# Performance work log

Hardware: AMD Instinct MI355X
Metric: run time of the kernel (lower is better)

## Reference

```python
import jax, jax.numpy as jnp
import numpy as np

BETA = 0.001
VAR_MIN = 1e-7


def setup_inputs() -> dict:
    key = jax.random.key(0)
    ks = jax.random.split(key, 16)
    B, IN, N, Z, S = 2048, 32, 1024, 8, 8
    f32 = jnp.float32
    return {
        "batch": jax.random.normal(ks[0], (B, IN, N, 2), f32),
        "labels": jax.random.randint(ks[1], (B, 1), 0, 2).astype(jnp.int32),
        "eps1": jax.random.normal(ks[2], (B, S, Z), f32),
        "eps2": jax.random.normal(ks[3], (B, S, Z), f32),
        "W1": jax.random.normal(ks[4], (IN, 32), f32) / np.sqrt(IN),
        "b1": jax.random.normal(ks[5], (32,), f32) * 0.01,
        "W2": jax.random.normal(ks[6], (32, 32), f32) / np.sqrt(32),
        "b2": jax.random.normal(ks[7], (32,), f32) * 0.01,
        "Wmu": jax.random.normal(ks[8], (32, Z), f32) / np.sqrt(32),
        "bmu": jax.random.normal(ks[9], (Z,), f32) * 0.01,
        "Wv": jax.random.normal(ks[10], (32, Z), f32) / np.sqrt(32),
        "bv": jax.random.normal(ks[11], (Z,), f32) * 0.01,
        "sw": jax.random.normal(ks[12], (1, 1), f32),
        "sb": jax.random.normal(ks[13], (1,), f32),
    }


def _cal_z(data, W1, b1, W2, b2, Wmu, bmu, Wv, bv):
    # data: [B, IN, N] -> points [B, N, IN]
    x = jnp.transpose(data, (0, 2, 1))
    h = jax.nn.relu(x @ W1 + b1)
    h = jax.nn.relu(h @ W2 + b2)
    mu = h @ Wmu + bmu                    # [B, N, Z]
    var = jax.nn.softplus(h @ Wv + bv)    # [B, N, Z]
    var = jnp.maximum(var, VAR_MIN)
    var_pog = 1.0 / jnp.sum(1.0 / var, axis=1)  # [B, Z]
    # Faithful to torch source: var is reassigned before mu update, so
    # mu = var_pog * sum(mu / var_pog) == sum(mu) over the N axis.
    mu_pog = jnp.sum(mu, axis=1)                # [B, Z]
    return mu_pog, var_pog


def _kl(mu, var):
    # KL(N(mu, sqrt(var)) || N(0, 1)), elementwise, then mean
    return jnp.mean(-0.5 * jnp.log(var) + 0.5 * (var + mu * mu) - 0.5)


def reference(batch, labels, eps1, eps2, W1, b1, W2, b2, Wmu, bmu, Wv, bv, sw, sb):
    mu1, var1 = _cal_z(batch[:, :, :, 0], W1, b1, W2, b2, Wmu, bmu, Wv, bv)
    mu2, var2 = _cal_z(batch[:, :, :, 1], W1, b1, W2, b2, Wmu, bmu, Wv, bv)

    kl = (_kl(mu1, var1) + _kl(mu2, var2)) * BETA

    # rsample: mu + sigma * eps, [B, S, Z]
    z1 = mu1[:, None, :] + jnp.sqrt(var1)[:, None, :] * eps1
    z2 = mu2[:, None, :] + jnp.sqrt(var2)[:, None, :] * eps2

    # pairwise distances over the S x S sample grid: [B, S, S]
    diff = z1[:, :, None, :] - z2[:, None, :, :]
    dist = jnp.sqrt(jnp.sum(diff * diff, axis=-1))

    a = jax.nn.softplus(sw[0, 0])
    p = jax.nn.sigmoid(-a * dist + sb[0])
    loss1 = -jnp.log(p)
    loss_1 = jnp.mean(loss1, axis=(1, 2), keepdims=False)[:, None]  # [B, 1]
    # Faithful bug in torch source: loss0 is never assigned, stays zero,
    # so the (1 - labels) term contributes nothing.
    labels_f = labels.astype(loss_1.dtype)
    soft = jnp.mean(loss_1 * labels_f)

    return kl + soft
```

## Files before the change

### kernel.cpp

```cpp
#include <hip/hip_runtime.h>
#include <hip/hip_bf16.h>

#define B_   2048
#define N_   1024
#define BETA 0.001f
#define VAR_MIN 1e-7f

#define PTS   64
#define NSTG  (N_ / PTS)
#define RF    128
#define NBUF  3

typedef __attribute__((ext_vector_type(8))) short  bf16x8;
typedef __attribute__((ext_vector_type(4))) float  f32x4;

__device__ __forceinline__ unsigned short f2bf_u(float x) {
    __hip_bfloat16 h = __float2bfloat16(x);
    return __builtin_bit_cast(unsigned short, h);
}
__device__ __forceinline__ float softplus_cheap(float x) {
    float sp = __logf(1.f + __expf(x));
    return x > 15.f ? x : sp;
}
__device__ __forceinline__ float rcp_fast(float x) {
    return __builtin_amdgcn_rcpf(x);
}
__device__ __forceinline__ float softplus_ref(float x) {
    return x > 20.f ? x : log1pf(expf(x));
}

__device__ __forceinline__ int kperm(int k) {
    return 4 * (k >> 3) + (k & 3) + 16 * ((k >> 2) & 1);
}

extern "C" __global__ void hib_prep(const float* __restrict__ W1,
                                    const float* __restrict__ W2,
                                    const float* __restrict__ Wmu,
                                    const float* __restrict__ Wv,
                                    unsigned short* __restrict__ wf)
{
    const int l = threadIdx.x;
    const int r = l & 15, kb = l >> 4;
#pragma unroll
    for (int j = 0; j < 8; j++) {
        const int k1 = kb * 8 + j;
        const int kp = kperm(k1);
        wf[(0 * 64 + l) * 8 + j] = f2bf_u(W1[k1 * 32 + r]);
        wf[(1 * 64 + l) * 8 + j] = f2bf_u(W1[k1 * 32 + 16 + r]);
        wf[(2 * 64 + l) * 8 + j] = f2bf_u(W2[kp * 32 + r]);
        wf[(3 * 64 + l) * 8 + j] = f2bf_u(W2[kp * 32 + 16 + r]);
        wf[(4 * 64 + l) * 8 + j] = f2bf_u(r < 8 ? Wmu[kp * 8 + r]
                                                : Wv[kp * 8 + (r - 8)]);
    }
}

__device__ __forceinline__ bf16x8 pack_relu(f32x4 a, f32x4 b) {
    bf16x8 o;
    o[0] = (short)f2bf_u(fmaxf(a[0], 0.f));
    o[1] = (short)f2bf_u(fmaxf(a[1], 0.f));
    o[2] = (short)f2bf_u(fmaxf(a[2], 0.f));
    o[3] = (short)f2bf_u(fmaxf(a[3], 0.f));
    o[4] = (short)f2bf_u(fmaxf(b[0], 0.f));
    o[5] = (short)f2bf_u(fmaxf(b[1], 0.f));
    o[6] = (short)f2bf_u(fmaxf(b[2], 0.f));
    o[7] = (short)f2bf_u(fmaxf(b[3], 0.f));
    return o;
}

__device__ __forceinline__ void red16(f32x4& v) {
#pragma unroll
    for (int off = 8; off; off >>= 1) {
        v[0] += __shfl_down(v[0], off);
        v[1] += __shfl_down(v[1], off);
        v[2] += __shfl_down(v[2], off);
        v[3] += __shfl_down(v[3], off);
    }
}

__device__ __forceinline__ void stage_issue(const float* __restrict__ bbase,
                                            float* __restrict__ ldsbuf,
                                            int st, int wid, int l)
{
    const int sub = l >> 5, lo = l & 31;
#pragma unroll
    for (int q = 0; q < 4; ++q) {
        const int row = wid * 8 + q * 2;
        const float* gs = bbase + (size_t)(row + sub) * (2 * N_) + st * RF + lo * 4;
        __builtin_amdgcn_global_load_lds(
            (const __attribute__((address_space(1))) unsigned int*)gs,
            (__attribute__((address_space(3))) unsigned int*)&ldsbuf[row * RF],
            16, 0, 0);
    }
}

__global__ void __launch_bounds__(256, 3)
hib_mfma(const float* __restrict__ batch,
         const int* __restrict__ labels,
         const float* __restrict__ eps1, const float* __restrict__ eps2,
         const unsigned short* __restrict__ wf,
         const float* __restrict__ b1, const float* __restrict__ b2,
         const float* __restrict__ bmu, const float* __restrict__ bv,
         const float* __restrict__ sw, const float* __restrict__ sb,
         float* __restrict__ out)
{
    __shared__ float lds[NBUF][32 * RF];
    __shared__ float sacc[32];

    const int tid = threadIdx.x;
    const int b   = blockIdx.x;
    const int wid = tid >> 6, l = tid & 63;
    const int c   = l & 15, kb = l >> 4;

    if (tid < 32) sacc[tid] = 0.f;

    const bf16x8* wfv = (const bf16x8*)wf;
    const bf16x8 A1a = wfv[0 * 64 + l], A1b = wfv[1 * 64 + l];
    const bf16x8 A2a = wfv[2 * 64 + l], A2b = wfv[3 * 64 + l];
    const bf16x8 Ahd = wfv[4 * 64 + l];

    const int r4 = 4 * kb;
    const bool is_v = (kb >= 2);
    const int  z4   = 4 * (kb & 1);
    f32x4 c1a, c1b, c2a, c2b, chd;
    c1a[0] = b1[r4];      c1a[1] = b1[r4 + 1];      c1a[2] = b1[r4 + 2];      c1a[3] = b1[r4 + 3];
    c1b[0] = b1[16 + r4]; c1b[1] = b1[16 + r4 + 1]; c1b[2] = b1[16 + r4 + 2]; c1b[3] = b1[16 + r4 + 3];
    c2a[0] = b2[r4];      c2a[1] = b2[r4 + 1];      c2a[2] = b2[r4 + 2];      c2a[3] = b2[r4 + 3];
    c2b[0] = b2[16 + r4]; c2b[1] = b2[16 + r4 + 1]; c2b[2] = b2[16 + r4 + 2]; c2b[3] = b2[16 + r4 + 3];
    if (is_v) { chd[0] = bv[z4];  chd[1] = bv[z4 + 1];  chd[2] = bv[z4 + 2];  chd[3] = bv[z4 + 3]; }
    else      { chd[0] = bmu[z4]; chd[1] = bmu[z4 + 1]; chd[2] = bmu[z4 + 2]; chd[3] = bmu[z4 + 3]; }

    f32x4 acc0 = {0.f, 0.f, 0.f, 0.f};
    f32x4 acc1 = {0.f, 0.f, 0.f, 0.f};

    const float* bbase = batch + (size_t)b * 32 * (2 * N_);

    stage_issue(bbase, lds[0], 0, wid, l);
    stage_issue(bbase, lds[1], 1, wid, l);
    asm volatile("s_waitcnt vmcnt(4)" ::: "memory");
    __builtin_amdgcn_s_barrier();
    __builtin_amdgcn_sched_barrier(0);

#pragma unroll 1
    for (int t = 0; t < NSTG; ++t) {
        const int cur = t % NBUF;
        if (t + 2 < NSTG)
            stage_issue(bbase, lds[(t + 2) % NBUF], t + 2, wid, l);

        float2 xr[8];
#pragma unroll
        for (int j = 0; j < 8; j++)
            xr[j] = *(const float2*)&lds[cur][(kb * 8 + j) * RF + (wid * 16 + c) * 2];

        bf16x8 f0, f1;
#pragma unroll
        for (int j = 0; j < 8; j++) {
            f0[j] = (short)f2bf_u(xr[j].x);
            f1[j] = (short)f2bf_u(xr[j].y);
        }

        f32x4 d1a0 = __builtin_amdgcn_mfma_f32_16x16x32_bf16(A1a, f0, c1a, 0, 0, 0);
        f32x4 d1b0 = __builtin_amdgcn_mfma_f32_16x16x32_bf16(A1b, f0, c1b, 0, 0, 0);
        f32x4 d1a1 = __builtin_amdgcn_mfma_f32_16x16x32_bf16(A1a, f1, c1a, 0, 0, 0);
        f32x4 d1b1 = __builtin_amdgcn_mfma_f32_16x16x32_bf16(A1b, f1, c1b, 0, 0, 0);

        bf16x8 p20 = pack_relu(d1a0, d1b0);
        bf16x8 p21 = pack_relu(d1a1, d1b1);

        f32x4 d2a0 = __builtin_amdgcn_mfma_f32_16x16x32_bf16(A2a, p20, c2a, 0, 0, 0);
        f32x4 d2b0 = __builtin_amdgcn_mfma_f32_16x16x32_bf16(A2b, p20, c2b, 0, 0, 0);
        f32x4 d2a1 = __builtin_amdgcn_mfma_f32_16x16x32_bf16(A2a, p21, c2a, 0, 0, 0);
        f32x4 d2b1 = __builtin_amdgcn_mfma_f32_16x16x32_bf16(A2b, p21, c2b, 0, 0, 0);

        bf16x8 p30 = pack_relu(d2a0, d2b0);
        bf16x8 p31 = pack_relu(d2a1, d2b1);

        f32x4 e0 = __builtin_amdgcn_mfma_f32_16x16x32_bf16(Ahd, p30, chd, 0, 0, 0);
        f32x4 e1 = __builtin_amdgcn_mfma_f32_16x16x32_bf16(Ahd, p31, chd, 0, 0, 0);

        if (!is_v) {
            acc0[0] += e0[0]; acc0[1] += e0[1]; acc0[2] += e0[2]; acc0[3] += e0[3];
            acc1[0] += e1[0]; acc1[1] += e1[1]; acc1[2] += e1[2]; acc1[3] += e1[3];
        } else {
            acc0[0] += rcp_fast(fmaxf(softplus_cheap(e0[0]), VAR_MIN));
            acc0[1] += rcp_fast(fmaxf(softplus_cheap(e0[1]), VAR_MIN));
            acc0[2] += rcp_fast(fmaxf(softplus_cheap(e0[2]), VAR_MIN));
            acc0[3] += rcp_fast(fmaxf(softplus_cheap(e0[3]), VAR_MIN));
            acc1[0] += rcp_fast(fmaxf(softplus_cheap(e1[0]), VAR_MIN));
            acc1[1] += rcp_fast(fmaxf(softplus_cheap(e1[1]), VAR_MIN));
            acc1[2] += rcp_fast(fmaxf(softplus_cheap(e1[2]), VAR_MIN));
            acc1[3] += rcp_fast(fmaxf(softplus_cheap(e1[3]), VAR_MIN));
        }

        if (t + 2 < NSTG)
            asm volatile("s_waitcnt vmcnt(4)" ::: "memory");
        else
            asm volatile("s_waitcnt vmcnt(0)" ::: "memory");
        __builtin_amdgcn_s_barrier();
        __builtin_amdgcn_sched_barrier(0);
    }

    red16(acc0);
    red16(acc1);

    if (c == 0) {
        const int base = (is_v ? 16 : 0) + z4;
        atomicAdd(&sacc[base + 0],     acc0[0]);
        atomicAdd(&sacc[base + 1],     acc0[1]);
        atomicAdd(&sacc[base + 2],     acc0[2]);
        atomicAdd(&sacc[base + 3],     acc0[3]);
        atomicAdd(&sacc[base + 8 + 0], acc1[0]);
        atomicAdd(&sacc[base + 8 + 1], acc1[1]);
        atomicAdd(&sacc[base + 8 + 2], acc1[2]);
        atomicAdd(&sacc[base + 8 + 3], acc1[3]);
    }
    __syncthreads();

    if (tid < 64) {
        const float a    = softplus_ref(sw[0]);
        const float sbv_ = sb[0];

        float muA[8], muB[8], sgA[8], sgB[8];
#pragma unroll
        for (int z = 0; z < 8; z++) {
            muA[z] = sacc[z];
            muB[z] = sacc[8 + z];
            sgA[z] = sqrtf(1.0f / sacc[16 + z]);
            sgB[z] = sqrtf(1.0f / sacc[24 + z]);
        }
        const int i = tid >> 3, j = tid & 7;
        float d2 = 0.f;
#pragma unroll
        for (int z = 0; z < 8; z++) {
            float e1 = eps1[((size_t)b * 8 + i) * 8 + z];
            float e2 = eps2[((size_t)b * 8 + j) * 8 + z];
            float zz1 = fmaf(sgA[z], e1, muA[z]);
            float zz2 = fmaf(sgB[z], e2, muB[z]);
            float d = zz1 - zz2;
            d2 = fmaf(d, d, d2);
        }
        const float lab = (float)labels[b];
        float contrib = softplus_ref(a * sqrtf(d2) - sbv_) * lab
                      * (1.0f / (64.0f * (float)B_));

        if (tid < 16) {
            const int cc = tid >> 3, z = tid & 7;
            float iv  = sacc[16 + cc * 8 + z];
            float var = 1.0f / iv;
            float m   = sacc[cc * 8 + z];
            contrib += (-0.5f * logf(var) + 0.5f * (var + m * m) - 0.5f)
                       * (BETA / (8.0f * (float)B_));
        }
#pragma unroll
        for (int off = 32; off; off >>= 1) contrib += __shfl_down(contrib, off);
        if (tid == 0) atomicAdd(out, contrib);
    }
}

extern "C" void kernel_launch(void* const* d_in, const int* in_sizes, int n_in,
                              void* d_out, int out_size, void* d_ws, size_t ws_size,
                              hipStream_t stream)
{
    (void)in_sizes; (void)n_in; (void)out_size; (void)ws_size;
    const float* batch  = (const float*)d_in[0];
    const int*   labels = (const int*)  d_in[1];
    const float* eps1   = (const float*)d_in[2];
    const float* eps2   = (const float*)d_in[3];
    const float* W1     = (const float*)d_in[4];
    const float* b1     = (const float*)d_in[5];
    const float* W2     = (const float*)d_in[6];
    const float* b2     = (const float*)d_in[7];
    const float* Wmu    = (const float*)d_in[8];
    const float* bmu    = (const float*)d_in[9];
    const float* Wv     = (const float*)d_in[10];
    const float* bv     = (const float*)d_in[11];
    const float* sw     = (const float*)d_in[12];
    const float* sb     = (const float*)d_in[13];

    unsigned short* wf = (unsigned short*)d_ws;

    hipMemsetAsync(d_out, 0, sizeof(float), stream);
    hib_prep<<<1, 64, 0, stream>>>(W1, W2, Wmu, Wv, wf);
    hib_mfma<<<B_, 256, 0, stream>>>(batch, labels, eps1, eps2, wf,
                                     b1, b2, bmu, bv, sw, sb, (float*)d_out);
}
```

Before: 140.8 us.

## Split input channels into two half-chunks with double-buffered LDS and masked layer-1 MFMA

```diff
diff --git a/kernel.cpp b/kernel.cpp
--- a/kernel.cpp
+++ b/kernel.cpp
@@ -5,11 +5,7 @@
 #define N_   1024
 #define BETA 0.001f
 #define VAR_MIN 1e-7f
-
-#define PTS   64
-#define NSTG  (N_ / PTS)
-#define RF    128
-#define NBUF  3
+#define NP   8
 
 typedef __attribute__((ext_vector_type(8))) short  bf16x8;
 typedef __attribute__((ext_vector_type(4))) float  f32x4;
@@ -78,22 +74,43 @@
 }
 
 __device__ __forceinline__ void stage_issue(const float* __restrict__ bbase,
-                                            float* __restrict__ ldsbuf,
-                                            int st, int wid, int l)
-{
-    const int sub = l >> 5, lo = l & 31;
+                                            float* __restrict__ buf,
+                                            int chunk, int P, int wid, int l)
+{
 #pragma unroll
     for (int q = 0; q < 4; ++q) {
-        const int row = wid * 8 + q * 2;
-        const float* gs = bbase + (size_t)(row + sub) * (2 * N_) + st * RF + lo * 4;
+        const int rl = wid * 4 + q;
+        const float* gs = bbase + (size_t)(chunk * 16 + rl) * (2 * N_)
+                        + P * 256 + l * 4;
         __builtin_amdgcn_global_load_lds(
             (const __attribute__((address_space(1))) unsigned int*)gs,
-            (__attribute__((address_space(3))) unsigned int*)&ldsbuf[row * RF],
+            (__attribute__((address_space(3))) unsigned int*)&buf[rl * 256],
             16, 0, 0);
     }
 }
 
-__global__ void __launch_bounds__(256, 3)
+__device__ __forceinline__ void load_pack(const float* __restrict__ buf,
+                                          int p, int wid, int c, int kb,
+                                          bool active, bf16x8& f0, bf16x8& f1)
+{
+    const int rbase = (kb & 1) * 8;
+    const int col   = (p * 64 + wid * 16 + c) * 2;
+    float2 xr[8];
+#pragma unroll
+    for (int j = 0; j < 8; ++j)
+        xr[j] = *(const float2*)&buf[(rbase + j) * 256 + col];
+    bf16x8 t0, t1;
+#pragma unroll
+    for (int j = 0; j < 8; ++j) {
+        t0[j] = (short)f2bf_u(xr[j].x);
+        t1[j] = (short)f2bf_u(xr[j].y);
+    }
+    const bf16x8 z = {0, 0, 0, 0, 0, 0, 0, 0};
+    f0 = active ? t0 : z;
+    f1 = active ? t1 : z;
+}
+
+__global__ void __launch_bounds__(256, 4)
 hib_mfma(const float* __restrict__ batch,
          const int* __restrict__ labels,
          const float* __restrict__ eps1, const float* __restrict__ eps2,
@@ -103,7 +120,7 @@
          const float* __restrict__ sw, const float* __restrict__ sb,
          float* __restrict__ out)
 {
-    __shared__ float lds[NBUF][32 * RF];
+    __shared__ float lds[2][16 * 256];
     __shared__ float sacc[32];
 
     const int tid = threadIdx.x;
@@ -134,69 +151,73 @@
 
     const float* bbase = batch + (size_t)b * 32 * (2 * N_);
 
-    stage_issue(bbase, lds[0], 0, wid, l);
-    stage_issue(bbase, lds[1], 1, wid, l);
-    asm volatile("s_waitcnt vmcnt(4)" ::: "memory");
-    __builtin_amdgcn_s_barrier();
-    __builtin_amdgcn_sched_barrier(0);
+    stage_issue(bbase, lds[0], 0, 0, wid, l);
 
 #pragma unroll 1
-    for (int t = 0; t < NSTG; ++t) {
-        const int cur = t % NBUF;
-        if (t + 2 < NSTG)
-            stage_issue(bbase, lds[(t + 2) % NBUF], t + 2, wid, l);
-
-        float2 xr[8];
-#pragma unroll
-        for (int j = 0; j < 8; j++)
-            xr[j] = *(const float2*)&lds[cur][(kb * 8 + j) * RF + (wid * 16 + c) * 2];
-
-        bf16x8 f0, f1;
-#pragma unroll
-        for (int j = 0; j < 8; j++) {
-            f0[j] = (short)f2bf_u(xr[j].x);
-            f1[j] = (short)f2bf_u(xr[j].y);
-        }
-
-        f32x4 d1a0 = __builtin_amdgcn_mfma_f32_16x16x32_bf16(A1a, f0, c1a, 0, 0, 0);
-        f32x4 d1b0 = __builtin_amdgcn_mfma_f32_16x16x32_bf16(A1b, f0, c1b, 0, 0, 0);
-        f32x4 d1a1 = __builtin_amdgcn_mfma_f32_16x16x32_bf16(A1a, f1, c1a, 0, 0, 0);
-        f32x4 d1b1 = __builtin_amdgcn_mfma_f32_16x16x32_bf16(A1b, f1, c1b, 0, 0, 0);
-
-        bf16x8 p20 = pack_relu(d1a0, d1b0);
-        bf16x8 p21 = pack_relu(d1a1, d1b1);
-
-        f32x4 d2a0 = __builtin_amdgcn_mfma_f32_16x16x32_bf16(A2a, p20, c2a, 0, 0, 0);
-        f32x4 d2b0 = __builtin_amdgcn_mfma_f32_16x16x32_bf16(A2b, p20, c2b, 0, 0, 0);
-        f32x4 d2a1 = __builtin_amdgcn_mfma_f32_16x16x32_bf16(A2a, p21, c2a, 0, 0, 0);
-        f32x4 d2b1 = __builtin_amdgcn_mfma_f32_16x16x32_bf16(A2b, p21, c2b, 0, 0, 0);
-
-        bf16x8 p30 = pack_relu(d2a0, d2b0);
-        bf16x8 p31 = pack_relu(d2a1, d2b1);
-
-        f32x4 e0 = __builtin_amdgcn_mfma_f32_16x16x32_bf16(Ahd, p30, chd, 0, 0, 0);
-        f32x4 e1 = __builtin_amdgcn_mfma_f32_16x16x32_bf16(Ahd, p31, chd, 0, 0, 0);
-
-        if (!is_v) {
-            acc0[0] += e0[0]; acc0[1] += e0[1]; acc0[2] += e0[2]; acc0[3] += e0[3];
-            acc1[0] += e1[0]; acc1[1] += e1[1]; acc1[2] += e1[2]; acc1[3] += e1[3];
-        } else {
-            acc0[0] += rcp_fast(fmaxf(softplus_cheap(e0[0]), VAR_MIN));
-            acc0[1] += rcp_fast(fmaxf(softplus_cheap(e0[1]), VAR_MIN));
-            acc0[2] += rcp_fast(fmaxf(softplus_cheap(e0[2]), VAR_MIN));
-            acc0[3] += rcp_fast(fmaxf(softplus_cheap(e0[3]), VAR_MIN));
-            acc1[0] += rcp_fast(fmaxf(softplus_cheap(e1[0]), VAR_MIN));
-            acc1[1] += rcp_fast(fmaxf(softplus_cheap(e1[1]), VAR_MIN));
-            acc1[2] += rcp_fast(fmaxf(softplus_cheap(e1[2]), VAR_MIN));
-            acc1[3] += rcp_fast(fmaxf(softplus_cheap(e1[3]), VAR_MIN));
-        }
-
-        if (t + 2 < NSTG)
-            asm volatile("s_waitcnt vmcnt(4)" ::: "memory");
-        else
-            asm volatile("s_waitcnt vmcnt(0)" ::: "memory");
+    for (int P = 0; P < NP; ++P) {
+        f32x4 hA[2], hB[2], hC[2], hD[2];
+
+        stage_issue(bbase, lds[1], 1, P, wid, l);
+        asm volatile("s_waitcnt vmcnt(4)" ::: "memory");
         __builtin_amdgcn_s_barrier();
         __builtin_amdgcn_sched_barrier(0);
+#pragma unroll
+        for (int p = 0; p < 2; ++p) {
+            bf16x8 f0, f1;
+            load_pack(lds[0], p, wid, c, kb, kb < 2, f0, f1);
+            hA[p] = __builtin_amdgcn_mfma_f32_16x16x32_bf16(A1a, f0, c1a, 0, 0, 0);
+            hB[p] = __builtin_amdgcn_mfma_f32_16x16x32_bf16(A1b, f0, c1b, 0, 0, 0);
+            hC[p] = __builtin_amdgcn_mfma_f32_16x16x32_bf16(A1a, f1, c1a, 0, 0, 0);
+            hD[p] = __builtin_amdgcn_mfma_f32_16x16x32_bf16(A1b, f1, c1b, 0, 0, 0);
+        }
+        __builtin_amdgcn_s_barrier();
+
+        if (P + 1 < NP) {
+            stage_issue(bbase, lds[0], 0, P + 1, wid, l);
+            asm volatile("s_waitcnt vmcnt(4)" ::: "memory");
+        } else {
+            asm volatile("s_waitcnt vmcnt(0)" ::: "memory");
+        }
+        __builtin_amdgcn_s_barrier();
+        __builtin_amdgcn_sched_barrier(0);
+#pragma unroll
+        for (int p = 0; p < 2; ++p) {
+            bf16x8 f0, f1;
+            load_pack(lds[1], p, wid, c, kb, kb >= 2, f0, f1);
+            hA[p] = __builtin_amdgcn_mfma_f32_16x16x32_bf16(A1a, f0, hA[p], 0, 0, 0);
+            hB[p] = __builtin_amdgcn_mfma_f32_16x16x32_bf16(A1b, f0, hB[p], 0, 0, 0);
+            hC[p] = __builtin_amdgcn_mfma_f32_16x16x32_bf16(A1a, f1, hC[p], 0, 0, 0);
+            hD[p] = __builtin_amdgcn_mfma_f32_16x16x32_bf16(A1b, f1, hD[p], 0, 0, 0);
+
+            bf16x8 p20 = pack_relu(hA[p], hB[p]);
+            bf16x8 p21 = pack_relu(hC[p], hD[p]);
+
+            f32x4 d2a0 = __builtin_amdgcn_mfma_f32_16x16x32_bf16(A2a, p20, c2a, 0, 0, 0);
+            f32x4 d2b0 = __builtin_amdgcn_mfma_f32_16x16x32_bf16(A2b, p20, c2b, 0, 0, 0);
+            f32x4 d2a1 = __builtin_amdgcn_mfma_f32_16x16x32_bf16(A2a, p21, c2a, 0, 0, 0);
+            f32x4 d2b1 = __builtin_amdgcn_mfma_f32_16x16x32_bf16(A2b, p21, c2b, 0, 0, 0);
+
+            bf16x8 p30 = pack_relu(d2a0, d2b0);
+            bf16x8 p31 = pack_relu(d2a1, d2b1);
+
+            f32x4 e0 = __builtin_amdgcn_mfma_f32_16x16x32_bf16(Ahd, p30, chd, 0, 0, 0);
+            f32x4 e1 = __builtin_amdgcn_mfma_f32_16x16x32_bf16(Ahd, p31, chd, 0, 0, 0);
+
+            if (!is_v) {
+                acc0[0] += e0[0]; acc0[1] += e0[1]; acc0[2] += e0[2]; acc0[3] += e0[3];
+                acc1[0] += e1[0]; acc1[1] += e1[1]; acc1[2] += e1[2]; acc1[3] += e1[3];
+            } else {
+                acc0[0] += rcp_fast(fmaxf(softplus_cheap(e0[0]), VAR_MIN));
+                acc0[1] += rcp_fast(fmaxf(softplus_cheap(e0[1]), VAR_MIN));
+                acc0[2] += rcp_fast(fmaxf(softplus_cheap(e0[2]), VAR_MIN));
+                acc0[3] += rcp_fast(fmaxf(softplus_cheap(e0[3]), VAR_MIN));
+                acc1[0] += rcp_fast(fmaxf(softplus_cheap(e1[0]), VAR_MIN));
+                acc1[1] += rcp_fast(fmaxf(softplus_cheap(e1[1]), VAR_MIN));
+                acc1[2] += rcp_fast(fmaxf(softplus_cheap(e1[2]), VAR_MIN));
+                acc1[3] += rcp_fast(fmaxf(softplus_cheap(e1[3]), VAR_MIN));
+            }
+        }
+        __builtin_amdgcn_s_barrier();
     }
 
     red16(acc0);
```

New measurement: 141.2 us. About the same (+0.3%).
